# Optimization experiments

Hardware: AMD Instinct MI355X
Metric: run time of the kernel (lower is better)

## Reference

```python
import jax, jax.numpy as jnp
import numpy as np

NEG_SLOPE = 0.01  # torch F.leaky_relu default


def setup_inputs() -> dict:
    key = jax.random.key(0)
    k1, k2, k3, k4, k5 = jax.random.split(key, 5)
    N, E, IN_DIM, OUT_DIM = 100000, 1600000, 128, 64
    h = jax.random.normal(k1, (N, IN_DIM), dtype=jnp.float32)
    src = jax.random.randint(k2, (E,), 0, N, dtype=jnp.int64)
    dst = jax.random.randint(k3, (E,), 0, N, dtype=jnp.int64)
    # xavier_normal-ish scaled params
    W1 = jax.random.normal(k4, (OUT_DIM, IN_DIM), dtype=jnp.float32) * (2.0 / (IN_DIM + OUT_DIM)) ** 0.5
    Wa = jax.random.normal(k5, (1, 2 * OUT_DIM), dtype=jnp.float32) * (2.0 / (2 * OUT_DIM + 1)) ** 0.5
    return {"h": h, "src": src, "dst": dst, "W1": W1, "Wa": Wa}


def reference(h, src, dst, W1, Wa):
    N = h.shape[0]
    D = W1.shape[0]
    z = h @ W1.T  # [N, D]
    z_src = z[src]  # [E, D] gather
    z_dst = z[dst]  # [E, D] gather
    a_src, a_dst = Wa[0, :D], Wa[0, D:]
    # attn_fc(concat(z_src, z_dst)) == z_src@a_src + z_dst@a_dst
    e = z_src @ a_src + z_dst @ a_dst  # [E]
    e = jnp.where(e >= 0, e, NEG_SLOPE * e)  # leaky_relu
    # segment softmax over incoming edges of each dst node
    e_max = jax.ops.segment_max(e, dst, num_segments=N)
    e_max = jnp.where(jnp.isfinite(e_max), e_max, 0.0)  # empty segments
    e_exp = jnp.exp(e - e_max[dst])
    denom = jax.ops.segment_sum(e_exp, dst, num_segments=N)
    alpha = e_exp / jnp.maximum(denom, 1e-16)[dst]  # [E]
    # weighted scatter-sum of source messages
    h_out = jax.ops.segment_sum(alpha[:, None] * z_src, dst, num_segments=N)  # [N, D]
    return h_out
```

## Files before the change

kernel.cpp:

```cpp
#include <hip/hip_runtime.h>
#include <hip/hip_bf16.h>

#define NEG_SLOPE 0.01f
#define NPB 512
#define CHUNK 4096

typedef __attribute__((ext_vector_type(8))) short short8;
typedef __attribute__((ext_vector_type(4))) float f32x4;

__device__ __forceinline__ unsigned short f2bf_rne(float f) {
    unsigned u = __float_as_uint(f);
    u += 0x7FFFu + ((u >> 16) & 1u);
    return (unsigned short)(u >> 16);
}

__global__ __launch_bounds__(256) void k_gp(
    const float* __restrict__ h, const float* __restrict__ W1,
    const float* __restrict__ Wa, unsigned short* __restrict__ zb,
    float* __restrict__ s, float* __restrict__ t, int N, int G1,
    const int* __restrict__ src, const int* __restrict__ dst,
    unsigned* __restrict__ gcur, unsigned* __restrict__ table,
    int E, int NBKT, int BCAP)
{
    __shared__ __align__(16) union SM {
        struct { short hsb[64 * 128]; short wsb[64 * 128]; } g;
        struct {
            unsigned cnt[256]; unsigned exc[256]; unsigned sbuf[256];
            unsigned gbaseb[256]; unsigned stage[CHUNK];
            unsigned short bkt[CHUNK];
        } p;
    } sm;
    const int tid = threadIdx.x;

    if (blockIdx.x < (unsigned)G1) {
        const int nb = blockIdx.x * 64;
        const float4* __restrict__ h4 = (const float4*)h;
        const float4* __restrict__ W14 = (const float4*)W1;
#pragma unroll
        for (int it = 0; it < 4; ++it) {
            const int q = tid + it * 256;
            const int r = q >> 4, cb = q & 15;
            const int sidx = r * 128 + ((cb * 8) ^ ((r & 7) << 3));
            {
                const int n = nb + r;
                float4 v0 = make_float4(0.f,0.f,0.f,0.f), v1 = v0;
                if (n < N) { v0 = h4[(size_t)n * 32 + cb * 2]; v1 = h4[(size_t)n * 32 + cb * 2 + 1]; }
                short8 o;
                o[0]=f2bf_rne(v0.x); o[1]=f2bf_rne(v0.y); o[2]=f2bf_rne(v0.z); o[3]=f2bf_rne(v0.w);
                o[4]=f2bf_rne(v1.x); o[5]=f2bf_rne(v1.y); o[6]=f2bf_rne(v1.z); o[7]=f2bf_rne(v1.w);
                *(short8*)&sm.g.hsb[sidx] = o;
            }
            {
                float4 v0 = W14[(size_t)r * 32 + cb * 2];
                float4 v1 = W14[(size_t)r * 32 + cb * 2 + 1];
                short8 o;
                o[0]=f2bf_rne(v0.x); o[1]=f2bf_rne(v0.y); o[2]=f2bf_rne(v0.z); o[3]=f2bf_rne(v0.w);
                o[4]=f2bf_rne(v1.x); o[5]=f2bf_rne(v1.y); o[6]=f2bf_rne(v1.z); o[7]=f2bf_rne(v1.w);
                *(short8*)&sm.g.wsb[sidx] = o;
            }
        }
        __syncthreads();

        const int w  = tid >> 6;
        const int l  = tid & 63;
        const int lr = l & 15;
        const int lc = l >> 4;
        f32x4 acc[4];
#pragma unroll
        for (int ni = 0; ni < 4; ++ni) acc[ni] = (f32x4){0.f, 0.f, 0.f, 0.f};

#pragma unroll
        for (int ks = 0; ks < 4; ++ks) {
            const int kcb = ks * 4 + lc;
            const short8 af = *(const short8*)&sm.g.hsb[(w * 16 + lr) * 128 + ((kcb * 8) ^ ((lr & 7) << 3))];
#pragma unroll
            for (int ni = 0; ni < 4; ++ni) {
                const int wr = ni * 16 + lr;
                const short8 bf = *(const short8*)&sm.g.wsb[wr * 128 + ((kcb * 8) ^ ((wr & 7) << 3))];
                acc[ni] = __builtin_amdgcn_mfma_f32_16x16x32_bf16(af, bf, acc[ni], 0, 0, 0);
            }
        }

        float asrc[4], adst[4];
#pragma unroll
        for (int ni = 0; ni < 4; ++ni) {
            asrc[ni] = Wa[ni * 16 + lr];
            adst[ni] = Wa[64 + ni * 16 + lr];
        }
#pragma unroll
        for (int r = 0; r < 4; ++r) {
            float ps = 0.f, pt = 0.f;
#pragma unroll
            for (int ni = 0; ni < 4; ++ni) {
                ps = fmaf(acc[ni][r], asrc[ni], ps);
                pt = fmaf(acc[ni][r], adst[ni], pt);
            }
#pragma unroll
            for (int m = 1; m < 16; m <<= 1) {
                ps += __shfl_xor(ps, m);
                pt += __shfl_xor(pt, m);
            }
            const int node = nb + w * 16 + lc * 4 + r;
            if (lr == 0 && node < N) { s[node] = ps; t[node] = pt; }
        }
#pragma unroll
        for (int ni = 0; ni < 4; ++ni)
#pragma unroll
            for (int r = 0; r < 4; ++r) {
                const int node = nb + w * 16 + lc * 4 + r;
                if (node < N) zb[(size_t)node * 64 + ni * 16 + lr] = f2bf_rne(acc[ni][r]);
            }
    } else {
        const int e0 = (blockIdx.x - G1) * CHUNK;
        const int nE = min(CHUNK, E - e0);

        sm.p.cnt[tid] = 0u;
        __syncthreads();
        for (int i = tid; i < nE; i += 256)
            atomicAdd(&sm.p.cnt[(unsigned)dst[e0 + i] >> 9], 1u);
        __syncthreads();

        const unsigned myc = sm.p.cnt[tid];
        if (tid < NBKT && myc > 0u) sm.p.gbaseb[tid] = atomicAdd(&gcur[tid], myc);

        sm.p.sbuf[tid] = myc;
        __syncthreads();
        for (int off = 1; off < 256; off <<= 1) {
            unsigned x = (tid >= off) ? sm.p.sbuf[tid - off] : 0u;
            __syncthreads();
            sm.p.sbuf[tid] += x;
            __syncthreads();
        }
        sm.p.exc[tid] = sm.p.sbuf[tid] - myc;
        __syncthreads();
        sm.p.cnt[tid] = 0u;
        __syncthreads();

        for (int i = tid; i < nE; i += 256) {
            const unsigned d = (unsigned)dst[e0 + i];
            const unsigned b = d >> 9;
            const unsigned pos = sm.p.exc[b] + atomicAdd(&sm.p.cnt[b], 1u);
            sm.p.stage[pos] = ((unsigned)src[e0 + i] << 9) | (d & 511u);
            sm.p.bkt[pos] = (unsigned short)b;
        }
        __syncthreads();

        for (int i = tid; i < nE; i += 256) {
            const unsigned b = sm.p.bkt[i];
            const unsigned off = sm.p.gbaseb[b] + ((unsigned)i - sm.p.exc[b]);
            if (off < (unsigned)BCAP)
                table[(size_t)b * BCAP + off] = sm.p.stage[i];
        }
    }
}

__global__ __launch_bounds__(256) void k_scanb(
    const unsigned* __restrict__ gcur, unsigned* __restrict__ gbase,
    int NBKT, int BCAP)
{
    __shared__ unsigned sbuf[256];
    const int t = threadIdx.x;
    unsigned c = (t < NBKT) ? min(gcur[t], (unsigned)BCAP) : 0u;
    sbuf[t] = c;
    __syncthreads();
    for (int off = 1; off < 256; off <<= 1) {
        unsigned x = (t >= off) ? sbuf[t - off] : 0u;
        __syncthreads();
        sbuf[t] += x;
        __syncthreads();
    }
    if (t < NBKT) gbase[t] = sbuf[t] - c;
}

__global__ __launch_bounds__(256) void k_sortb2(
    const unsigned* __restrict__ table, const unsigned* __restrict__ gcur,
    const unsigned* __restrict__ gbase, unsigned* __restrict__ edge_src,
    unsigned* __restrict__ offsets, unsigned* __restrict__ counts,
    int N, int BCAP)
{
    __shared__ unsigned ncnt[NPB];
    __shared__ unsigned nexc[NPB];
    __shared__ unsigned sbuf[NPB];
    const int b = blockIdx.x;
    const int t = threadIdx.x;
    const int bc = min((int)gcur[b], BCAP);
    const unsigned base = gbase[b];
    const size_t tb = (size_t)b * BCAP;

    ncnt[t] = 0u; ncnt[t + 256] = 0u;
    __syncthreads();
    for (int i = t; i < bc; i += 256)
        atomicAdd(&ncnt[table[tb + i] & 511u], 1u);
    __syncthreads();

    const unsigned c0 = ncnt[t], c1 = ncnt[t + 256];
    sbuf[t] = c0; sbuf[t + 256] = c1;
    __syncthreads();
    for (int off = 1; off < NPB; off <<= 1) {
        unsigned x0 = (t >= off) ? sbuf[t - off] : 0u;
        unsigned x1 = (t + 256 >= off) ? sbuf[t + 256 - off] : 0u;
        __syncthreads();
        sbuf[t] += x0; sbuf[t + 256] += x1;
        __syncthreads();
    }
    nexc[t] = sbuf[t] - c0; nexc[t + 256] = sbuf[t + 256] - c1;
    __syncthreads();

    {
        const int n0 = b * NPB + t, n1 = n0 + 256;
        if (n0 < N) { offsets[n0] = base + nexc[t];        counts[n0] = c0; }
        if (n1 < N) { offsets[n1] = base + nexc[t + 256];  counts[n1] = c1; }
    }
    ncnt[t] = 0u; ncnt[t + 256] = 0u;
    __syncthreads();

    for (int i = t; i < bc; i += 256) {
        const unsigned v = table[tb + i];
        const unsigned l = v & 511u;
        const unsigned pos = nexc[l] + atomicAdd(&ncnt[l], 1u);
        edge_src[base + pos] = v >> 9;
    }
}

__global__ __launch_bounds__(256) void k_node(
    const unsigned* __restrict__ offsets, const unsigned* __restrict__ counts,
    const unsigned* __restrict__ edge_src,
    const float* __restrict__ s, const float* __restrict__ t,
    const unsigned short* __restrict__ zb, float* __restrict__ out, int N)
{
    const int tid = threadIdx.x;
    const int node = blockIdx.x * 16 + (tid >> 4);
    if (node >= N) return;
    const int wl    = tid & 63;
    const int gbase = wl & ~15;
    const int sub   = wl & 15;
    const int g2    = sub >> 3;
    const int l8    = sub & 7;

    const unsigned beg = offsets[node];
    const int cnt = (int)counts[node];
    if (cnt == 0) {
        if (sub < 8) {
            const float4 zz = make_float4(0.f, 0.f, 0.f, 0.f);
            *(float4*)&out[(size_t)node * 64 + sub * 8]     = zz;
            *(float4*)&out[(size_t)node * 64 + sub * 8 + 4] = zz;
        }
        return;
    }

    const float tn = t[node];
    const unsigned short* __restrict__ zrow = zb + l8 * 8;
    float dl = 0.f;
    float acc[8] = {0.f, 0.f, 0.f, 0.f, 0.f, 0.f, 0.f, 0.f};

    for (int base = 0; base < cnt; base += 16) {
        const int rem = min(16, cnt - base);
        int sj = 0;
        float p = 0.f;
        if (sub < rem) {
            sj = (int)edge_src[beg + base + sub];
            float e = s[sj] + tn;
            e = (e >= 0.f) ? e : NEG_SLOPE * e;
            p = __expf(e);
            dl += p;
        }
#pragma unroll
        for (int k = 0; k < 8; ++k) {
            const int j = g2 * 8 + k;
            const float pj  = __shfl(p, gbase + j);
            const int   sjj = __shfl(sj, gbase + j);
            const uint4 v = *(const uint4*)&zrow[(size_t)sjj * 64];
#define UNPK(u, d0) \
            acc[d0]     = fmaf(pj, __uint_as_float((u) << 16),          acc[d0]); \
            acc[d0 + 1] = fmaf(pj, __uint_as_float((u) & 0xFFFF0000u), acc[d0 + 1]);
            UNPK(v.x, 0) UNPK(v.y, 2) UNPK(v.z, 4) UNPK(v.w, 6)
#undef UNPK
        }
    }

#pragma unroll
    for (int c = 0; c < 8; ++c)
        acc[c] += __shfl_xor(acc[c], 8);
    float den = dl;
#pragma unroll
    for (int m = 1; m < 16; m <<= 1) den += __shfl_xor(den, m);

    if (sub < 8) {
        const float inv = 1.f / fmaxf(den, 1e-16f);
        float4 o0 = make_float4(acc[0] * inv, acc[1] * inv, acc[2] * inv, acc[3] * inv);
        float4 o1 = make_float4(acc[4] * inv, acc[5] * inv, acc[6] * inv, acc[7] * inv);
        *(float4*)&out[(size_t)node * 64 + sub * 8]     = o0;
        *(float4*)&out[(size_t)node * 64 + sub * 8 + 4] = o1;
    }
}

extern "C" void kernel_launch(void* const* d_in, const int* in_sizes, int n_in,
                              void* d_out, int out_size, void* d_ws, size_t ws_size,
                              hipStream_t stream) {
    const float* h   = (const float*)d_in[0];
    const int*   src = (const int*)d_in[1];
    const int*   dst = (const int*)d_in[2];
    const float* W1  = (const float*)d_in[3];
    const float* Wa  = (const float*)d_in[4];
    float* out = (float*)d_out;

    const int N = in_sizes[0] / 128;
    const int E = in_sizes[1];
    const int NBKT = (N + NPB - 1) / NPB;
    const int meanb = (E + NBKT - 1) / NBKT;
    int slack = 24 * (int)sqrtf((float)meanb) + 64;
    const int BCAP = meanb + slack;

    const int G1 = (N + 63) / 64;
    const int G2 = (E + CHUNK - 1) / CHUNK;

    unsigned short* zb = (unsigned short*)d_ws;
    float*    s        = (float*)(zb + (size_t)N * 64);
    float*    t        = s + N;
    unsigned* gcur     = (unsigned*)(t + N);
    unsigned* gbase    = gcur + NBKT;
    unsigned* offsets  = gbase + NBKT;
    unsigned* counts   = offsets + N;
    unsigned* edge_src = counts + N;
    unsigned* table    = edge_src + E;

    hipMemsetAsync(gcur, 0, (size_t)NBKT * sizeof(unsigned), stream);

    k_gp<<<G1 + G2, 256, 0, stream>>>(h, W1, Wa, zb, s, t, N, G1,
                                      src, dst, gcur, table, E, NBKT, BCAP);
    k_scanb<<<1, 256, 0, stream>>>(gcur, gbase, NBKT, BCAP);
    k_sortb2<<<NBKT, 256, 0, stream>>>(table, gcur, gbase, edge_src, offsets, counts, N, BCAP);
    k_node<<<(N + 15) / 16, 256, 0, stream>>>(offsets, counts, edge_src, s, t, zb, out, N);
}
```

Before: 105.3 us.

## Load h directly into MFMA registers, coalesce z stores, fold bucket scan into sort

The GEMM part of k_gp now loads h rows straight into registers as MFMA A-fragments instead of staging them in shared memory, which halves the LDS footprint. It adds launch_bounds occupancy 4 and stages the bf16 z output through LDS so each row is written with 16-byte stores instead of scattered 2-byte stores. The separate single-block k_scanb launch is removed; each k_sortb2 block redoes the 196-entry bucket prefix scan itself. This saves one kernel launch and its serialization, at the cost of redundant scans and extra barriers in each sort block.

After: 103.9 us. Within noise of the previous version (-1.4%).

```diff
diff --git a/kernel.cpp b/kernel.cpp
--- a/kernel.cpp
+++ b/kernel.cpp
@@ -14,7 +14,7 @@
     return (unsigned short)(u >> 16);
 }
 
-__global__ __launch_bounds__(256) void k_gp(
+__global__ __launch_bounds__(256, 4) void k_gp(
     const float* __restrict__ h, const float* __restrict__ W1,
     const float* __restrict__ Wa, unsigned short* __restrict__ zb,
     float* __restrict__ s, float* __restrict__ t, int N, int G1,
@@ -23,7 +23,7 @@
     int E, int NBKT, int BCAP)
 {
     __shared__ __align__(16) union SM {
-        struct { short hsb[64 * 128]; short wsb[64 * 128]; } g;
+        short wsb[64 * 128];
         struct {
             unsigned cnt[256]; unsigned exc[256]; unsigned sbuf[256];
             unsigned gbaseb[256]; unsigned stage[CHUNK];
@@ -34,82 +34,109 @@
 
     if (blockIdx.x < (unsigned)G1) {
         const int nb = blockIdx.x * 64;
-        const float4* __restrict__ h4 = (const float4*)h;
-        const float4* __restrict__ W14 = (const float4*)W1;
-#pragma unroll
-        for (int it = 0; it < 4; ++it) {
-            const int q = tid + it * 256;
-            const int r = q >> 4, cb = q & 15;
-            const int sidx = r * 128 + ((cb * 8) ^ ((r & 7) << 3));
-            {
-                const int n = nb + r;
-                float4 v0 = make_float4(0.f,0.f,0.f,0.f), v1 = v0;
-                if (n < N) { v0 = h4[(size_t)n * 32 + cb * 2]; v1 = h4[(size_t)n * 32 + cb * 2 + 1]; }
-                short8 o;
-                o[0]=f2bf_rne(v0.x); o[1]=f2bf_rne(v0.y); o[2]=f2bf_rne(v0.z); o[3]=f2bf_rne(v0.w);
-                o[4]=f2bf_rne(v1.x); o[5]=f2bf_rne(v1.y); o[6]=f2bf_rne(v1.z); o[7]=f2bf_rne(v1.w);
-                *(short8*)&sm.g.hsb[sidx] = o;
-            }
-            {
-                float4 v0 = W14[(size_t)r * 32 + cb * 2];
-                float4 v1 = W14[(size_t)r * 32 + cb * 2 + 1];
-                short8 o;
-                o[0]=f2bf_rne(v0.x); o[1]=f2bf_rne(v0.y); o[2]=f2bf_rne(v0.z); o[3]=f2bf_rne(v0.w);
-                o[4]=f2bf_rne(v1.x); o[5]=f2bf_rne(v1.y); o[6]=f2bf_rne(v1.z); o[7]=f2bf_rne(v1.w);
-                *(short8*)&sm.g.wsb[sidx] = o;
-            }
-        }
-        __syncthreads();
-
         const int w  = tid >> 6;
         const int l  = tid & 63;
         const int lr = l & 15;
         const int lc = l >> 4;
-        f32x4 acc[4];
-#pragma unroll
-        for (int ni = 0; ni < 4; ++ni) acc[ni] = (f32x4){0.f, 0.f, 0.f, 0.f};
-
+        const int myn = nb + w * 16 + lr;
+        const float4* __restrict__ h4 = (const float4*)h;
+        const float4* __restrict__ W14 = (const float4*)W1;
+
+        float4 av[4][2];
 #pragma unroll
         for (int ks = 0; ks < 4; ++ks) {
             const int kcb = ks * 4 + lc;
-            const short8 af = *(const short8*)&sm.g.hsb[(w * 16 + lr) * 128 + ((kcb * 8) ^ ((lr & 7) << 3))];
+            if (myn < N) {
+                av[ks][0] = h4[(size_t)myn * 32 + kcb * 2];
+                av[ks][1] = h4[(size_t)myn * 32 + kcb * 2 + 1];
+            } else {
+                av[ks][0] = make_float4(0.f, 0.f, 0.f, 0.f);
+                av[ks][1] = make_float4(0.f, 0.f, 0.f, 0.f);
+            }
+        }
+
+#pragma unroll
+        for (int it = 0; it < 4; ++it) {
+            const int q = tid + it * 256;
+            const int r = q >> 4, cb = q & 15;
+            float4 v0 = W14[(size_t)r * 32 + cb * 2];
+            float4 v1 = W14[(size_t)r * 32 + cb * 2 + 1];
+            short8 o;
+            o[0]=f2bf_rne(v0.x); o[1]=f2bf_rne(v0.y); o[2]=f2bf_rne(v0.z); o[3]=f2bf_rne(v0.w);
+            o[4]=f2bf_rne(v1.x); o[5]=f2bf_rne(v1.y); o[6]=f2bf_rne(v1.z); o[7]=f2bf_rne(v1.w);
+            *(short8*)&sm.wsb[r * 128 + ((cb * 8) ^ ((r & 7) << 3))] = o;
+        }
+        __syncthreads();
+
+        f32x4 acc[4];
+#pragma unroll
+        for (int ni = 0; ni < 4; ++ni) acc[ni] = (f32x4){0.f, 0.f, 0.f, 0.f};
+
+#pragma unroll
+        for (int ks = 0; ks < 4; ++ks) {
+            const int kcb = ks * 4 + lc;
+            short8 af;
+            af[0]=f2bf_rne(av[ks][0].x); af[1]=f2bf_rne(av[ks][0].y);
+            af[2]=f2bf_rne(av[ks][0].z); af[3]=f2bf_rne(av[ks][0].w);
+            af[4]=f2bf_rne(av[ks][1].x); af[5]=f2bf_rne(av[ks][1].y);
+            af[6]=f2bf_rne(av[ks][1].z); af[7]=f2bf_rne(av[ks][1].w);
 #pragma unroll
             for (int ni = 0; ni < 4; ++ni) {
                 const int wr = ni * 16 + lr;
-                const short8 bf = *(const short8*)&sm.g.wsb[wr * 128 + ((kcb * 8) ^ ((wr & 7) << 3))];
+                const short8 bf = *(const short8*)&sm.wsb[wr * 128 + ((kcb * 8) ^ ((wr & 7) << 3))];
                 acc[ni] = __builtin_amdgcn_mfma_f32_16x16x32_bf16(af, bf, acc[ni], 0, 0, 0);
             }
         }
 
-        float asrc[4], adst[4];
+        {
+            float asrc[4], adst[4];
+#pragma unroll
+            for (int ni = 0; ni < 4; ++ni) {
+                asrc[ni] = Wa[ni * 16 + lr];
+                adst[ni] = Wa[64 + ni * 16 + lr];
+            }
+#pragma unroll
+            for (int r = 0; r < 4; ++r) {
+                float ps = 0.f, pt = 0.f;
+#pragma unroll
+                for (int ni = 0; ni < 4; ++ni) {
+                    ps = fmaf(acc[ni][r], asrc[ni], ps);
+                    pt = fmaf(acc[ni][r], adst[ni], pt);
+                }
+#pragma unroll
+                for (int m = 1; m < 16; m <<= 1) {
+                    ps += __shfl_xor(ps, m);
+                    pt += __shfl_xor(pt, m);
+                }
+                const int node = nb + w * 16 + lc * 4 + r;
+                if (lr == 0 && node < N) { s[node] = ps; t[node] = pt; }
+            }
+        }
+
+        __syncthreads();
 #pragma unroll
         for (int ni = 0; ni < 4; ++ni) {
-            asrc[ni] = Wa[ni * 16 + lr];
-            adst[ni] = Wa[64 + ni * 16 + lr];
-        }
-#pragma unroll
-        for (int r = 0; r < 4; ++r) {
-            float ps = 0.f, pt = 0.f;
-#pragma unroll
-            for (int ni = 0; ni < 4; ++ni) {
-                ps = fmaf(acc[ni][r], asrc[ni], ps);
-                pt = fmaf(acc[ni][r], adst[ni], pt);
-            }
-#pragma unroll
-            for (int m = 1; m < 16; m <<= 1) {
-                ps += __shfl_xor(ps, m);
-                pt += __shfl_xor(pt, m);
-            }
-            const int node = nb + w * 16 + lc * 4 + r;
-            if (lr == 0 && node < N) { s[node] = ps; t[node] = pt; }
-        }
-#pragma unroll
-        for (int ni = 0; ni < 4; ++ni)
+            const int col = ni * 16 + lr;
 #pragma unroll
             for (int r = 0; r < 4; ++r) {
-                const int node = nb + w * 16 + lc * 4 + r;
-                if (node < N) zb[(size_t)node * 64 + ni * 16 + lr] = f2bf_rne(acc[ni][r]);
-            }
+                const int row = w * 16 + lc * 4 + r;
+                sm.wsb[row * 64 + (((col >> 3) ^ (row & 7)) << 3) + (col & 7)]
+                    = (short)f2bf_rne(acc[ni][r]);
+            }
+        }
+        __syncthreads();
+        {
+            const int r = tid >> 2;
+            const int n = nb + r;
+            if (n < N) {
+#pragma unroll
+                for (int j = 0; j < 2; ++j) {
+                    const int c = (tid & 3) * 2 + j;
+                    const short8 v = *(const short8*)&sm.wsb[r * 64 + ((c ^ (r & 7)) << 3)];
+                    *(short8*)&zb[(size_t)n * 64 + c * 8] = v;
+                }
+            }
+        }
     } else {
         const int e0 = (blockIdx.x - G1) * CHUNK;
         const int nE = min(CHUNK, E - e0);
@@ -154,38 +181,36 @@
     }
 }
 
-__global__ __launch_bounds__(256) void k_scanb(
-    const unsigned* __restrict__ gcur, unsigned* __restrict__ gbase,
-    int NBKT, int BCAP)
-{
-    __shared__ unsigned sbuf[256];
-    const int t = threadIdx.x;
-    unsigned c = (t < NBKT) ? min(gcur[t], (unsigned)BCAP) : 0u;
-    sbuf[t] = c;
-    __syncthreads();
-    for (int off = 1; off < 256; off <<= 1) {
-        unsigned x = (t >= off) ? sbuf[t - off] : 0u;
-        __syncthreads();
-        sbuf[t] += x;
-        __syncthreads();
-    }
-    if (t < NBKT) gbase[t] = sbuf[t] - c;
-}
-
 __global__ __launch_bounds__(256) void k_sortb2(
     const unsigned* __restrict__ table, const unsigned* __restrict__ gcur,
-    const unsigned* __restrict__ gbase, unsigned* __restrict__ edge_src,
+    unsigned* __restrict__ edge_src,
     unsigned* __restrict__ offsets, unsigned* __restrict__ counts,
-    int N, int BCAP)
+    int N, int NBKT, int BCAP)
 {
     __shared__ unsigned ncnt[NPB];
     __shared__ unsigned nexc[NPB];
     __shared__ unsigned sbuf[NPB];
+    __shared__ unsigned basesh;
     const int b = blockIdx.x;
     const int t = threadIdx.x;
     const int bc = min((int)gcur[b], BCAP);
-    const unsigned base = gbase[b];
     const size_t tb = (size_t)b * BCAP;
+
+    {
+        unsigned c = (t < NBKT) ? min(gcur[t], (unsigned)BCAP) : 0u;
+        sbuf[t] = c;
+        __syncthreads();
+        for (int off = 1; off < 256; off <<= 1) {
+            unsigned x = (t >= off) ? sbuf[t - off] : 0u;
+            __syncthreads();
+            sbuf[t] += x;
+            __syncthreads();
+        }
+        if (t == 0) basesh = (b == 0) ? 0u : sbuf[b - 1];
+        __syncthreads();
+    }
+    const unsigned base = basesh;
+    __syncthreads();
 
     ncnt[t] = 0u; ncnt[t + 256] = 0u;
     __syncthreads();
@@ -318,8 +343,7 @@
     float*    s        = (float*)(zb + (size_t)N * 64);
     float*    t        = s + N;
     unsigned* gcur     = (unsigned*)(t + N);
-    unsigned* gbase    = gcur + NBKT;
-    unsigned* offsets  = gbase + NBKT;
+    unsigned* offsets  = gcur + NBKT;
     unsigned* counts   = offsets + N;
     unsigned* edge_src = counts + N;
     unsigned* table    = edge_src + E;
@@ -328,7 +352,6 @@
 
     k_gp<<<G1 + G2, 256, 0, stream>>>(h, W1, Wa, zb, s, t, N, G1,
                                       src, dst, gcur, table, E, NBKT, BCAP);
-    k_scanb<<<1, 256, 0, stream>>>(gcur, gbase, NBKT, BCAP);
-    k_sortb2<<<NBKT, 256, 0, stream>>>(table, gcur, gbase, edge_src, offsets, counts, N, BCAP);
+    k_sortb2<<<NBKT, 256, 0, stream>>>(table, gcur, edge_src, offsets, counts, N, NBKT, BCAP);
     k_node<<<(N + 15) / 16, 256, 0, stream>>>(offsets, counts, edge_src, s, t, zb, out, N);
 }
```
